# Kernel optimization log

Measured on AMD Instinct MI355X. Metric: run time of the kernel, lower is better.

The kernel has to match this reference:

```python
import jax, jax.numpy as jnp
import numpy as np

BZ, D_IN, D_STATE, D_OUT, L = 8, 256, 512, 256, 4096


def setup_inputs() -> dict:
    key = jax.random.key(0)
    k_u, k_a, k_b, k_c = jax.random.split(key, 4)
    init_scale = 0.5
    u = jax.random.normal(k_u, (BZ, D_IN, L), dtype=jnp.float32)
    A_unconstrained = jax.random.normal(k_a, (D_STATE,), dtype=jnp.float32) * 0.1
    B_mat = jax.random.normal(k_b, (D_STATE, D_IN), dtype=jnp.float32) * init_scale / np.sqrt(D_IN)
    C_mat = jax.random.normal(k_c, (D_OUT, D_STATE), dtype=jnp.float32) * init_scale / np.sqrt(D_STATE)
    D_mat = jnp.zeros((D_OUT, D_IN), dtype=jnp.float32)
    h0 = jnp.zeros((D_STATE,), dtype=jnp.float32)
    return {"u": u, "A_unconstrained": A_unconstrained, "B_mat": B_mat,
            "C_mat": C_mat, "D_mat": D_mat, "h0": h0}


def reference(u, A_unconstrained, B_mat, C_mat, D_mat, h0):
    # u: (B, input_dim, L)
    Bz = u.shape[0]
    A_diag = -jax.nn.softplus(A_unconstrained)          # (S,)
    # Precompute input projection for all timesteps: (L, B, S)
    Bu = jnp.einsum('bil,si->lbs', u, B_mat)
    state0 = jnp.broadcast_to(h0[None, :], (Bz, A_diag.shape[0]))

    def step(state, bu_t):
        x_t = state * A_diag[None, :] + bu_t            # (B, S)
        return x_t, x_t

    _, xs = jax.lax.scan(step, state0, Bu)              # xs: (L, B, S)
    # y_t = x_t @ C^T + u_t @ D^T, assembled as (B, output_dim, L)
    Y = jnp.einsum('lbs,os->bol', xs, C_mat) + jnp.einsum('bil,oi->bol', u, D_mat)
    return Y
```

## Files before the change

### kernel.cpp

```cpp
#include <hip/hip_runtime.h>
#include <math.h>

#define BZ 8
#define DI 256
#define DS 512
#define DOUT 256
#define LL 4096
#define BS (BZ * DS)
#define CH 64
#define CT 64
#define XST 520

typedef __bf16 bf16x8 __attribute__((ext_vector_type(8)));
typedef float f32x4 __attribute__((ext_vector_type(4)));
typedef unsigned short us8 __attribute__((ext_vector_type(8)));

#define WAITV(n) asm volatile("s_waitcnt vmcnt(" #n ")" ::: "memory")
#define WAITL0   asm volatile("s_waitcnt lgkmcnt(0)" ::: "memory")
#define SB0      __builtin_amdgcn_sched_barrier(0)

__device__ __forceinline__ ushort f2b(float f) {
    union { float f; unsigned u; } v; v.f = f;
    unsigned r = v.u + 0x7FFFu + ((v.u >> 16) & 1u);
    return (ushort)(r >> 16);
}
__device__ __forceinline__ float b2f(ushort h) {
    union { unsigned u; float f; } v; v.u = ((unsigned)h) << 16;
    return v.f;
}

__device__ __forceinline__ void gload16(const void* g, ushort* l) {
    __builtin_amdgcn_global_load_lds(
        (const __attribute__((address_space(1))) unsigned int*)g,
        (__attribute__((address_space(3))) unsigned int*)l,
        16, 0, 0);
}

__global__ __launch_bounds__(256) void k_prep(const float* __restrict__ Au,
                                              float* __restrict__ apow,
                                              const float* __restrict__ Bm,
                                              const float* __restrict__ Cm,
                                              ushort* __restrict__ Bmb,
                                              ushort* __restrict__ Cmb) {
    const int t = blockIdx.x * 256 + threadIdx.x;
    const int n1 = DS * DI / 4, n2 = DOUT * DS / 4;
    if (t < n1) {
        float4 v = ((const float4*)Bm)[t];
        ushort4 o; o.x = f2b(v.x); o.y = f2b(v.y); o.z = f2b(v.z); o.w = f2b(v.w);
        ((ushort4*)Bmb)[t] = o;
    } else if (t < n1 + n2) {
        float4 v = ((const float4*)Cm)[t - n1];
        ushort4 o; o.x = f2b(v.x); o.y = f2b(v.y); o.z = f2b(v.z); o.w = f2b(v.w);
        ((ushort4*)Cmb)[t - n1] = o;
    }
    if (t < DS) {
        float x = Au[t];
        float sp = (x > 15.f) ? x : log1pf(expf(x));
        float ad = -sp;
        float p = 1.f;
        apow[t] = 1.f;
        for (int j = 1; j <= CT; ++j) { p *= ad; apow[j * DS + t] = p; }
    }
}

__global__ __launch_bounds__(256) void k_finals(const float* __restrict__ u,
                                                const ushort* __restrict__ Bmb,
                                                const float* __restrict__ apow,
                                                float* __restrict__ finals) {
    __shared__ ushort smem[13312];
    const int tid = threadIdx.x;
    const int w = tid >> 6, lane = tid & 63;
    const int mrow = lane & 15, quad = lane >> 4;
    const int c0 = blockIdx.x, sg = blockIdx.y, b = blockIdx.z;
    const int s0 = sg * 128, l0 = c0 * 64;

    f32x4 acc[2][4];
#pragma unroll
    for (int mi = 0; mi < 2; ++mi)
#pragma unroll
        for (int ni = 0; ni < 4; ++ni) acc[mi][ni] = (f32x4)0.f;

    const float* usrc = u + ((size_t)b * DI + 4 * w + (lane >> 4)) * LL + l0 + (lane & 15) * 4;

    auto stageU = [&](int it) {
        const int bufu = (it & 1) * 4096;
        const float* s_ = usrc + (size_t)(it * 32) * LL;
        gload16(s_, smem + bufu + w * 512);
        gload16(s_ + (size_t)16 * LL, smem + bufu + w * 512 + 2048);
    };
    auto xposeU = [&](int it) {
        const float* uf = (const float*)&smem[(it & 1) * 4096];
        const int bto = 8192 + (it & 1) * 2560;
        float va[4], vb[4];
#pragma unroll
        for (int j = 0; j < 4; ++j) {
            va[j] = uf[(4 * w + j) * 64 + lane];
            vb[j] = uf[(16 + 4 * w + j) * 64 + lane];
        }
        ushort4 o1, o2;
        o1.x = f2b(va[0]); o1.y = f2b(va[1]); o1.z = f2b(va[2]); o1.w = f2b(va[3]);
        o2.x = f2b(vb[0]); o2.y = f2b(vb[1]); o2.z = f2b(vb[2]); o2.w = f2b(vb[3]);
        *(ushort4*)&smem[bto + lane * 40 + 4 * w] = o1;
        *(ushort4*)&smem[bto + lane * 40 + 16 + 4 * w] = o2;
    };

    stageU(0);
    __syncthreads();
#pragma unroll
    for (int it = 0; it < DI / 32; ++it) {
        if (it + 1 < DI / 32) stageU(it + 1);
        xposeU(it);
        __syncthreads();
        const int bto = 8192 + (it & 1) * 2560;
        bf16x8 bfr[4];
#pragma unroll
        for (int ni = 0; ni < 4; ++ni)
            bfr[ni] = *(const bf16x8*)&smem[bto + (ni * 16 + mrow) * 40 + quad * 8];
        bf16x8 af[2];
#pragma unroll
        for (int mi = 0; mi < 2; ++mi)
            af[mi] = *(const bf16x8*)&Bmb[(size_t)(s0 + 32 * w + mi * 16 + mrow) * DI + it * 32 + quad * 8];
#pragma unroll
        for (int mi = 0; mi < 2; ++mi)
#pragma unroll
            for (int ni = 0; ni < 4; ++ni)
                acc[mi][ni] = __builtin_amdgcn_mfma_f32_16x16x32_bf16(af[mi], bfr[ni], acc[mi][ni], 0, 0, 0);
        __syncthreads();
    }

    float F[2][4];
#pragma unroll
    for (int mi = 0; mi < 2; ++mi) {
        const int sb = s0 + 32 * w + mi * 16 + quad * 4;
        f32x4 a16 = *(const f32x4*)&apow[16 * DS + sb];
        f32x4 wgt = *(const f32x4*)&apow[(size_t)(15 - mrow) * DS + sb];
#pragma unroll
        for (int r = 0; r < 4; ++r) {
            float h = acc[mi][0][r];
            h = h * a16[r] + acc[mi][1][r];
            h = h * a16[r] + acc[mi][2][r];
            h = h * a16[r] + acc[mi][3][r];
            F[mi][r] = wgt[r] * h;
        }
    }
#pragma unroll
    for (int d = 1; d < 16; d <<= 1)
#pragma unroll
        for (int mi = 0; mi < 2; ++mi)
#pragma unroll
            for (int r = 0; r < 4; ++r)
                F[mi][r] += __shfl_xor(F[mi][r], d);
    if (mrow == 0) {
#pragma unroll
        for (int mi = 0; mi < 2; ++mi) {
            f32x4 o; o[0] = F[mi][0]; o[1] = F[mi][1]; o[2] = F[mi][2]; o[3] = F[mi][3];
            *(f32x4*)&finals[(size_t)c0 * BS + (size_t)b * DS + s0 + 32 * w + mi * 16 + quad * 4] = o;
        }
    }
}

__global__ __launch_bounds__(256, 2) void k_mainB(const float* __restrict__ u,
                                                  const ushort* __restrict__ Bmb,
                                                  const ushort* __restrict__ Cmb,
                                                  const float* __restrict__ apow,
                                                  const float* __restrict__ h0,
                                                  const float* __restrict__ finals,
                                                  float* __restrict__ Y) {
    __shared__ ushort smem[34304];
    float* crl = (float*)&smem[33280];
    const int tid = threadIdx.x;
    const int w = tid >> 6, lane = tid & 63;
    const int mrow = lane & 15, quad = lane >> 4;
    const int c0 = blockIdx.x, b = blockIdx.y;
    const int l0 = c0 * 64;

    const float* usrc = u + ((size_t)b * DI + 4 * w + (lane >> 4)) * LL + l0 + (lane & 15) * 4;

    auto stageU = [&](int it) {
        const int bufu = (it % 3) * 4096;
        const float* s_ = usrc + (size_t)(it * 32) * LL;
        gload16(s_, smem + bufu + w * 512);
        gload16(s_ + (size_t)16 * LL, smem + bufu + w * 512 + 2048);
    };
    auto xposeU = [&](int it) {
        const float* uf = (const float*)&smem[(it % 3) * 4096];
        const int bto = 12288 + (it & 1) * 2560;
        float va[4], vb[4];
#pragma unroll
        for (int j = 0; j < 4; ++j) {
            va[j] = uf[(4 * w + j) * 64 + lane];
            vb[j] = uf[(16 + 4 * w + j) * 64 + lane];
        }
        ushort4 o1, o2;
        o1.x = f2b(va[0]); o1.y = f2b(va[1]); o1.z = f2b(va[2]); o1.w = f2b(va[3]);
        o2.x = f2b(vb[0]); o2.y = f2b(vb[1]); o2.z = f2b(vb[2]); o2.w = f2b(vb[3]);
        *(ushort4*)&smem[bto + lane * 40 + 4 * w] = o1;
        *(ushort4*)&smem[bto + lane * 40 + 16 + 4 * w] = o2;
    };

    stageU(0); stageU(1);
    {
        const float aT0 = apow[CT * DS + tid];
        const float aT1 = apow[CT * DS + 256 + tid];
        float cva = h0[tid], cvb = h0[256 + tid];
        const float* fb = finals + (size_t)b * DS;
        int c = 0;
        for (; c + 8 <= c0; c += 8) {
            float fa[8], fc[8];
#pragma unroll
            for (int j = 0; j < 8; ++j) {
                fa[j] = fb[(size_t)(c + j) * BS + tid];
                fc[j] = fb[(size_t)(c + j) * BS + 256 + tid];
            }
#pragma unroll
            for (int j = 0; j < 8; ++j) {
                cva = aT0 * cva + fa[j];
                cvb = aT1 * cvb + fc[j];
            }
        }
        for (; c < c0; ++c) {
            cva = aT0 * cva + fb[(size_t)c * BS + tid];
            cvb = aT1 * cvb + fb[(size_t)c * BS + 256 + tid];
        }
        crl[tid] = cva; crl[256 + tid] = cvb;
    }

    f32x4 acc1[8][4];
#pragma unroll
    for (int mi = 0; mi < 8; ++mi)
#pragma unroll
        for (int ni = 0; ni < 4; ++ni) acc1[mi][ni] = (f32x4)0.f;

#pragma unroll
    for (int it = 0; it < DI / 32; ++it) {
        bf16x8 af[8];
#pragma unroll
        for (int mi = 0; mi < 8; ++mi)
            af[mi] = *(const bf16x8*)&Bmb[(size_t)(128 * w + mi * 16 + mrow) * DI + it * 32 + quad * 8];
        SB0;
        if (it + 2 < DI / 32) stageU(it + 2);
        if (it == 0) { WAITV(12); }
        xposeU(it);
        WAITL0;
        __builtin_amdgcn_s_barrier();
        SB0;
        const int bto = 12288 + (it & 1) * 2560;
        bf16x8 bfr[4];
#pragma unroll
        for (int ni = 0; ni < 4; ++ni)
            bfr[ni] = *(const bf16x8*)&smem[bto + (ni * 16 + mrow) * 40 + quad * 8];
#pragma unroll
        for (int mi = 0; mi < 8; ++mi)
#pragma unroll
            for (int ni = 0; ni < 4; ++ni)
                acc1[mi][ni] = __builtin_amdgcn_mfma_f32_16x16x32_bf16(af[mi], bfr[ni], acc1[mi][ni], 0, 0, 0);
        WAITL0;
        __builtin_amdgcn_s_barrier();
        SB0;
    }
    __syncthreads();

#pragma unroll
    for (int mi = 0; mi < 8; ++mi) {
        const int sloc = 128 * w + mi * 16 + quad * 4;
#pragma unroll
        for (int ni = 0; ni < 4; ++ni) {
            const int lloc = ni * 16 + mrow;
            f32x4 v = acc1[mi][ni];
            ushort4 o; o.x = f2b(v[0]); o.y = f2b(v[1]); o.z = f2b(v[2]); o.w = f2b(v[3]);
            *(ushort4*)&smem[lloc * XST + sloc] = o;
        }
    }
    __syncthreads();

    {
        const float2 av = *(const float2*)&apow[DS + 2 * tid];
        float x0 = 0.f, x1 = 0.f;
        unsigned* p = (unsigned*)&smem[2 * tid];
#pragma unroll 8
        for (int l = 0; l < CT; ++l) {
            unsigned v = p[l * (XST / 2)];
            x0 = av.x * x0 + b2f((ushort)(v & 0xFFFFu));
            x1 = av.y * x1 + b2f((ushort)(v >> 16));
            p[l * (XST / 2)] = (unsigned)f2b(x0) | ((unsigned)f2b(x1) << 16);
        }
    }
    __syncthreads();

    {
        const int lr = tid >> 2, g = tid & 3;
#pragma unroll
        for (int cc = 0; cc < 16; ++cc) {
            const int s = g * 128 + cc * 8;
            us8 x = *(const us8*)&smem[lr * XST + s];
            float4 a1 = *(const float4*)&apow[(size_t)(lr + 1) * DS + s];
            float4 a2 = *(const float4*)&apow[(size_t)(lr + 1) * DS + s + 4];
            float4 c1 = *(const float4*)&crl[s];
            float4 c2 = *(const float4*)&crl[s + 4];
            us8 o;
            o[0] = f2b(b2f(x[0]) + a1.x * c1.x);
            o[1] = f2b(b2f(x[1]) + a1.y * c1.y);
            o[2] = f2b(b2f(x[2]) + a1.z * c1.z);
            o[3] = f2b(b2f(x[3]) + a1.w * c1.w);
            o[4] = f2b(b2f(x[4]) + a2.x * c2.x);
            o[5] = f2b(b2f(x[5]) + a2.y * c2.y);
            o[6] = f2b(b2f(x[6]) + a2.z * c2.z);
            o[7] = f2b(b2f(x[7]) + a2.w * c2.w);
            *(us8*)&smem[lr * XST + s] = o;
        }
    }
    __syncthreads();

    f32x4 acc2[4][4];
#pragma unroll
    for (int mi = 0; mi < 4; ++mi)
#pragma unroll
        for (int ni = 0; ni < 4; ++ni) acc2[mi][ni] = (f32x4)0.f;

#pragma unroll
    for (int it = 0; it < DS / 32; ++it) {
        bf16x8 af2[4], bfr2[4];
#pragma unroll
        for (int mi = 0; mi < 4; ++mi)
            af2[mi] = *(const bf16x8*)&smem[(mi * 16 + mrow) * XST + it * 32 + quad * 8];
#pragma unroll
        for (int ni = 0; ni < 4; ++ni)
            bfr2[ni] = *(const bf16x8*)&Cmb[(size_t)(64 * w + ni * 16 + mrow) * DS + it * 32 + quad * 8];
#pragma unroll
        for (int mi = 0; mi < 4; ++mi)
#pragma unroll
            for (int ni = 0; ni < 4; ++ni)
                acc2[mi][ni] = __builtin_amdgcn_mfma_f32_16x16x32_bf16(af2[mi], bfr2[ni], acc2[mi][ni], 0, 0, 0);
    }

#pragma unroll
    for (int mi = 0; mi < 4; ++mi) {
        const int l = l0 + mi * 16 + quad * 4;
#pragma unroll
        for (int ni = 0; ni < 4; ++ni) {
            const int o = 64 * w + ni * 16 + mrow;
            *(float4*)&Y[((size_t)b * DOUT + o) * LL + l] = *(float4*)&acc2[mi][ni];
        }
    }
}

__global__ __launch_bounds__(256) void k_dadd(const float* __restrict__ Dm,
                                              const float* __restrict__ u,
                                              float* __restrict__ Y) {
    __shared__ int nz;
    if (threadIdx.x == 0) nz = 0;
    __syncthreads();
    const int o0 = blockIdx.x * 16;
    {
        const float4* dp = (const float4*)(Dm + (size_t)o0 * DI);
        int any = 0;
#pragma unroll
        for (int k = 0; k < 4; ++k) {
            float4 v = dp[threadIdx.x + k * 256];
            any |= (v.x != 0.f || v.y != 0.f || v.z != 0.f || v.w != 0.f);
        }
        if (any) atomicOr(&nz, 1);
    }
    __syncthreads();
    if (nz == 0) return;
    const int o = o0 + (threadIdx.x >> 4);
    const int li = threadIdx.x & 15;
    const int b = blockIdx.y;
    for (int lc = 0; lc < LL / 16; ++lc) {
        const int l = lc * 16 + li;
        float s = 0.f;
        for (int i = 0; i < DI; ++i)
            s += Dm[o * DI + i] * u[((size_t)b * DI + i) * LL + l];
        Y[((size_t)b * DOUT + o) * LL + l] += s;
    }
}

extern "C" void kernel_launch(void* const* d_in, const int* in_sizes, int n_in,
                              void* d_out, int out_size, void* d_ws, size_t ws_size,
                              hipStream_t stream) {
    const float* u  = (const float*)d_in[0];
    const float* Au = (const float*)d_in[1];
    const float* Bm = (const float*)d_in[2];
    const float* Cm = (const float*)d_in[3];
    const float* Dm = (const float*)d_in[4];
    const float* h0 = (const float*)d_in[5];
    float* Y = (float*)d_out;

    char* p = (char*)d_ws;
    float* finals  = (float*)p;  p += (size_t)CH * BS * 4;
    float* apow    = (float*)p;  p += (size_t)(CT + 1) * DS * 4;
    ushort* Bmb    = (ushort*)p; p += (size_t)DS * DI * 2;
    ushort* Cmb    = (ushort*)p; p += (size_t)DOUT * DS * 2;

    k_prep<<<dim3(256), 256, 0, stream>>>(Au, apow, Bm, Cm, Bmb, Cmb);
    k_finals<<<dim3(CH, DS / 128, BZ), 256, 0, stream>>>(u, Bmb, apow, finals);
    k_mainB<<<dim3(CH, BZ), 256, 0, stream>>>(u, Bmb, Cmb, apow, h0, finals, Y);
    k_dadd<<<dim3(DOUT / 16, BZ), 256, 0, stream>>>(Dm, u, Y);
}
```

Measured before the change: 163.3 us.

## Halve chunk length to 32 and restructure finals kernel to full-state tiles

The scan chunk length drops from 64 to 32 timesteps, which doubles the chunk count. k_mainB gets half-sized tiles and shared memory with higher occupancy, so the main kernel now runs 1024 blocks instead of 512. k_finals is reorganised so that each block covers all 512 states for a chunk, with a triple-buffered u pipeline and raw barriers replacing __syncthreads. The intra-chunk sequential scan is shorter and batches its LDS reads and writes in groups of 8. The cost is a longer serial prefix over finals in k_mainB (128 chunks instead of 64) and more finals traffic.

```diff
diff --git a/kernel.cpp b/kernel.cpp
--- a/kernel.cpp
+++ b/kernel.cpp
@@ -7,8 +7,8 @@
 #define DOUT 256
 #define LL 4096
 #define BS (BZ * DS)
-#define CH 64
-#define CT 64
+#define CH 128
+#define CT 32
 #define XST 520
 
 typedef __bf16 bf16x8 __attribute__((ext_vector_type(8)));
@@ -63,139 +63,123 @@
     }
 }
 
-__global__ __launch_bounds__(256) void k_finals(const float* __restrict__ u,
-                                                const ushort* __restrict__ Bmb,
-                                                const float* __restrict__ apow,
-                                                float* __restrict__ finals) {
-    __shared__ ushort smem[13312];
+__global__ __launch_bounds__(256, 4) void k_finals(const float* __restrict__ u,
+                                                   const ushort* __restrict__ Bmb,
+                                                   const float* __restrict__ apow,
+                                                   float* __restrict__ finals) {
+    __shared__ ushort smem[8704];
     const int tid = threadIdx.x;
     const int w = tid >> 6, lane = tid & 63;
     const int mrow = lane & 15, quad = lane >> 4;
-    const int c0 = blockIdx.x, sg = blockIdx.y, b = blockIdx.z;
-    const int s0 = sg * 128, l0 = c0 * 64;
-
-    f32x4 acc[2][4];
-#pragma unroll
-    for (int mi = 0; mi < 2; ++mi)
-#pragma unroll
-        for (int ni = 0; ni < 4; ++ni) acc[mi][ni] = (f32x4)0.f;
-
-    const float* usrc = u + ((size_t)b * DI + 4 * w + (lane >> 4)) * LL + l0 + (lane & 15) * 4;
+    const int c0 = blockIdx.x, b = blockIdx.y;
+    const int l0 = c0 * CT;
+
+    f32x4 acc[8][2];
+#pragma unroll
+    for (int mi = 0; mi < 8; ++mi)
+#pragma unroll
+        for (int ni = 0; ni < 2; ++ni) acc[mi][ni] = (f32x4)0.f;
+
+    const float* usrc = u + ((size_t)b * DI + (tid >> 3)) * LL + l0 + (tid & 7) * 4;
 
     auto stageU = [&](int it) {
-        const int bufu = (it & 1) * 4096;
-        const float* s_ = usrc + (size_t)(it * 32) * LL;
-        gload16(s_, smem + bufu + w * 512);
-        gload16(s_ + (size_t)16 * LL, smem + bufu + w * 512 + 2048);
+        gload16(usrc + (size_t)(it * 32) * LL, smem + (it % 3) * 2048 + w * 512);
     };
     auto xposeU = [&](int it) {
-        const float* uf = (const float*)&smem[(it & 1) * 4096];
-        const int bto = 8192 + (it & 1) * 2560;
-        float va[4], vb[4];
-#pragma unroll
-        for (int j = 0; j < 4; ++j) {
-            va[j] = uf[(4 * w + j) * 64 + lane];
-            vb[j] = uf[(16 + 4 * w + j) * 64 + lane];
-        }
-        ushort4 o1, o2;
-        o1.x = f2b(va[0]); o1.y = f2b(va[1]); o1.z = f2b(va[2]); o1.w = f2b(va[3]);
-        o2.x = f2b(vb[0]); o2.y = f2b(vb[1]); o2.z = f2b(vb[2]); o2.w = f2b(vb[3]);
-        *(ushort4*)&smem[bto + lane * 40 + 4 * w] = o1;
-        *(ushort4*)&smem[bto + lane * 40 + 16 + 4 * w] = o2;
+        const float* uf = (const float*)&smem[(it % 3) * 2048];
+        const int bto = 6144 + (it & 1) * 1280;
+        const int r0 = 8 * w + (lane >> 5) * 4, cl = lane & 31;
+        float v[4];
+#pragma unroll
+        for (int j = 0; j < 4; ++j) v[j] = uf[(r0 + j) * 32 + cl];
+        ushort4 o; o.x = f2b(v[0]); o.y = f2b(v[1]); o.z = f2b(v[2]); o.w = f2b(v[3]);
+        *(ushort4*)&smem[bto + cl * 40 + r0] = o;
     };
 
-    stageU(0);
-    __syncthreads();
+    stageU(0); stageU(1);
 #pragma unroll
     for (int it = 0; it < DI / 32; ++it) {
-        if (it + 1 < DI / 32) stageU(it + 1);
+        bf16x8 af[8];
+#pragma unroll
+        for (int mi = 0; mi < 8; ++mi)
+            af[mi] = *(const bf16x8*)&Bmb[(size_t)(128 * w + mi * 16 + mrow) * DI + it * 32 + quad * 8];
+        SB0;
+        if (it + 2 < DI / 32) stageU(it + 2);
+        if (it == 0) { WAITV(10); }
         xposeU(it);
-        __syncthreads();
-        const int bto = 8192 + (it & 1) * 2560;
-        bf16x8 bfr[4];
-#pragma unroll
-        for (int ni = 0; ni < 4; ++ni)
+        WAITL0;
+        __builtin_amdgcn_s_barrier();
+        SB0;
+        const int bto = 6144 + (it & 1) * 1280;
+        bf16x8 bfr[2];
+#pragma unroll
+        for (int ni = 0; ni < 2; ++ni)
             bfr[ni] = *(const bf16x8*)&smem[bto + (ni * 16 + mrow) * 40 + quad * 8];
-        bf16x8 af[2];
-#pragma unroll
-        for (int mi = 0; mi < 2; ++mi)
-            af[mi] = *(const bf16x8*)&Bmb[(size_t)(s0 + 32 * w + mi * 16 + mrow) * DI + it * 32 + quad * 8];
-#pragma unroll
-        for (int mi = 0; mi < 2; ++mi)
-#pragma unroll
-            for (int ni = 0; ni < 4; ++ni)
+#pragma unroll
+        for (int mi = 0; mi < 8; ++mi)
+#pragma unroll
+            for (int ni = 0; ni < 2; ++ni)
                 acc[mi][ni] = __builtin_amdgcn_mfma_f32_16x16x32_bf16(af[mi], bfr[ni], acc[mi][ni], 0, 0, 0);
-        __syncthreads();
-    }
-
-    float F[2][4];
-#pragma unroll
-    for (int mi = 0; mi < 2; ++mi) {
-        const int sb = s0 + 32 * w + mi * 16 + quad * 4;
+        WAITL0;
+        __builtin_amdgcn_s_barrier();
+        SB0;
+    }
+
+    float F[8][4];
+#pragma unroll
+    for (int mi = 0; mi < 8; ++mi) {
+        const int sb = 128 * w + mi * 16 + quad * 4;
         f32x4 a16 = *(const f32x4*)&apow[16 * DS + sb];
         f32x4 wgt = *(const f32x4*)&apow[(size_t)(15 - mrow) * DS + sb];
 #pragma unroll
-        for (int r = 0; r < 4; ++r) {
-            float h = acc[mi][0][r];
-            h = h * a16[r] + acc[mi][1][r];
-            h = h * a16[r] + acc[mi][2][r];
-            h = h * a16[r] + acc[mi][3][r];
-            F[mi][r] = wgt[r] * h;
-        }
+        for (int r = 0; r < 4; ++r)
+            F[mi][r] = wgt[r] * (acc[mi][0][r] * a16[r] + acc[mi][1][r]);
     }
 #pragma unroll
     for (int d = 1; d < 16; d <<= 1)
 #pragma unroll
-        for (int mi = 0; mi < 2; ++mi)
+        for (int mi = 0; mi < 8; ++mi)
 #pragma unroll
             for (int r = 0; r < 4; ++r)
                 F[mi][r] += __shfl_xor(F[mi][r], d);
     if (mrow == 0) {
 #pragma unroll
-        for (int mi = 0; mi < 2; ++mi) {
+        for (int mi = 0; mi < 8; ++mi) {
             f32x4 o; o[0] = F[mi][0]; o[1] = F[mi][1]; o[2] = F[mi][2]; o[3] = F[mi][3];
-            *(f32x4*)&finals[(size_t)c0 * BS + (size_t)b * DS + s0 + 32 * w + mi * 16 + quad * 4] = o;
-        }
-    }
-}
-
-__global__ __launch_bounds__(256, 2) void k_mainB(const float* __restrict__ u,
+            *(f32x4*)&finals[(size_t)c0 * BS + (size_t)b * DS + 128 * w + mi * 16 + quad * 4] = o;
+        }
+    }
+}
+
+__global__ __launch_bounds__(256, 4) void k_mainB(const float* __restrict__ u,
                                                   const ushort* __restrict__ Bmb,
                                                   const ushort* __restrict__ Cmb,
                                                   const float* __restrict__ apow,
                                                   const float* __restrict__ h0,
                                                   const float* __restrict__ finals,
                                                   float* __restrict__ Y) {
-    __shared__ ushort smem[34304];
-    float* crl = (float*)&smem[33280];
+    __shared__ ushort smem[17664];
+    float* crl = (float*)&smem[16640];
     const int tid = threadIdx.x;
     const int w = tid >> 6, lane = tid & 63;
     const int mrow = lane & 15, quad = lane >> 4;
     const int c0 = blockIdx.x, b = blockIdx.y;
-    const int l0 = c0 * 64;
-
-    const float* usrc = u + ((size_t)b * DI + 4 * w + (lane >> 4)) * LL + l0 + (lane & 15) * 4;
+    const int l0 = c0 * CT;
+
+    const float* usrc = u + ((size_t)b * DI + (tid >> 3)) * LL + l0 + (tid & 7) * 4;
 
     auto stageU = [&](int it) {
-        const int bufu = (it % 3) * 4096;
-        const float* s_ = usrc + (size_t)(it * 32) * LL;
-        gload16(s_, smem + bufu + w * 512);
-        gload16(s_ + (size_t)16 * LL, smem + bufu + w * 512 + 2048);
+        gload16(usrc + (size_t)(it * 32) * LL, smem + (it % 3) * 2048 + w * 512);
     };
     auto xposeU = [&](int it) {
-        const float* uf = (const float*)&smem[(it % 3) * 4096];
-        const int bto = 12288 + (it & 1) * 2560;
-        float va[4], vb[4];
-#pragma unroll
-        for (int j = 0; j < 4; ++j) {
-            va[j] = uf[(4 * w + j) * 64 + lane];
-            vb[j] = uf[(16 + 4 * w + j) * 64 + lane];
-        }
-        ushort4 o1, o2;
-        o1.x = f2b(va[0]); o1.y = f2b(va[1]); o1.z = f2b(va[2]); o1.w = f2b(va[3]);
-        o2.x = f2b(vb[0]); o2.y = f2b(vb[1]); o2.z = f2b(vb[2]); o2.w = f2b(vb[3]);
-        *(ushort4*)&smem[bto + lane * 40 + 4 * w] = o1;
-        *(ushort4*)&smem[bto + lane * 40 + 16 + 4 * w] = o2;
+        const float* uf = (const float*)&smem[(it % 3) * 2048];
+        const int bto = 6144 + (it & 1) * 1280;
+        const int r0 = 8 * w + (lane >> 5) * 4, cl = lane & 31;
+        float v[4];
+#pragma unroll
+        for (int j = 0; j < 4; ++j) v[j] = uf[(r0 + j) * 32 + cl];
+        ushort4 o; o.x = f2b(v[0]); o.y = f2b(v[1]); o.z = f2b(v[2]); o.w = f2b(v[3]);
+        *(ushort4*)&smem[bto + cl * 40 + r0] = o;
     };
 
     stageU(0); stageU(1);
@@ -225,11 +209,11 @@
         crl[tid] = cva; crl[256 + tid] = cvb;
     }
 
-    f32x4 acc1[8][4];
+    f32x4 acc1[8][2];
 #pragma unroll
     for (int mi = 0; mi < 8; ++mi)
 #pragma unroll
-        for (int ni = 0; ni < 4; ++ni) acc1[mi][ni] = (f32x4)0.f;
+        for (int ni = 0; ni < 2; ++ni) acc1[mi][ni] = (f32x4)0.f;
 
 #pragma unroll
     for (int it = 0; it < DI / 32; ++it) {
@@ -239,20 +223,20 @@
             af[mi] = *(const bf16x8*)&Bmb[(size_t)(128 * w + mi * 16 + mrow) * DI + it * 32 + quad * 8];
         SB0;
         if (it + 2 < DI / 32) stageU(it + 2);
-        if (it == 0) { WAITV(12); }
+        if (it == 0) { WAITV(10); }
         xposeU(it);
         WAITL0;
         __builtin_amdgcn_s_barrier();
         SB0;
-        const int bto = 12288 + (it & 1) * 2560;
-        bf16x8 bfr[4];
-#pragma unroll
-        for (int ni = 0; ni < 4; ++ni)
+        const int bto = 6144 + (it & 1) * 1280;
+        bf16x8 bfr[2];
+#pragma unroll
+        for (int ni = 0; ni < 2; ++ni)
             bfr[ni] = *(const bf16x8*)&smem[bto + (ni * 16 + mrow) * 40 + quad * 8];
 #pragma unroll
         for (int mi = 0; mi < 8; ++mi)
 #pragma unroll
-            for (int ni = 0; ni < 4; ++ni)
+            for (int ni = 0; ni < 2; ++ni)
                 acc1[mi][ni] = __builtin_amdgcn_mfma_f32_16x16x32_bf16(af[mi], bfr[ni], acc1[mi][ni], 0, 0, 0);
         WAITL0;
         __builtin_amdgcn_s_barrier();
@@ -264,7 +248,7 @@
     for (int mi = 0; mi < 8; ++mi) {
         const int sloc = 128 * w + mi * 16 + quad * 4;
 #pragma unroll
-        for (int ni = 0; ni < 4; ++ni) {
+        for (int ni = 0; ni < 2; ++ni) {
             const int lloc = ni * 16 + mrow;
             f32x4 v = acc1[mi][ni];
             ushort4 o; o.x = f2b(v[0]); o.y = f2b(v[1]); o.z = f2b(v[2]); o.w = f2b(v[3]);
@@ -276,22 +260,29 @@
     {
         const float2 av = *(const float2*)&apow[DS + 2 * tid];
         float x0 = 0.f, x1 = 0.f;
-        unsigned* p = (unsigned*)&smem[2 * tid];
-#pragma unroll 8
-        for (int l = 0; l < CT; ++l) {
-            unsigned v = p[l * (XST / 2)];
-            x0 = av.x * x0 + b2f((ushort)(v & 0xFFFFu));
-            x1 = av.y * x1 + b2f((ushort)(v >> 16));
-            p[l * (XST / 2)] = (unsigned)f2b(x0) | ((unsigned)f2b(x1) << 16);
+        unsigned* pp = (unsigned*)&smem[2 * tid];
+#pragma unroll
+        for (int bt = 0; bt < CT / 8; ++bt) {
+            unsigned v[8];
+#pragma unroll
+            for (int j = 0; j < 8; ++j) v[j] = pp[(bt * 8 + j) * (XST / 2)];
+#pragma unroll
+            for (int j = 0; j < 8; ++j) {
+                x0 = av.x * x0 + b2f((ushort)(v[j] & 0xFFFFu));
+                x1 = av.y * x1 + b2f((ushort)(v[j] >> 16));
+                v[j] = (unsigned)f2b(x0) | ((unsigned)f2b(x1) << 16);
+            }
+#pragma unroll
+            for (int j = 0; j < 8; ++j) pp[(bt * 8 + j) * (XST / 2)] = v[j];
         }
     }
     __syncthreads();
 
     {
-        const int lr = tid >> 2, g = tid & 3;
-#pragma unroll
-        for (int cc = 0; cc < 16; ++cc) {
-            const int s = g * 128 + cc * 8;
+        const int lr = tid >> 3, g = tid & 7;
+#pragma unroll
+        for (int cc = 0; cc < 8; ++cc) {
+            const int s = g * 64 + cc * 8;
             us8 x = *(const us8*)&smem[lr * XST + s];
             float4 a1 = *(const float4*)&apow[(size_t)(lr + 1) * DS + s];
             float4 a2 = *(const float4*)&apow[(size_t)(lr + 1) * DS + s + 4];
@@ -311,30 +302,30 @@
     }
     __syncthreads();
 
-    f32x4 acc2[4][4];
-#pragma unroll
-    for (int mi = 0; mi < 4; ++mi)
+    f32x4 acc2[2][4];
+#pragma unroll
+    for (int mi = 0; mi < 2; ++mi)
 #pragma unroll
         for (int ni = 0; ni < 4; ++ni) acc2[mi][ni] = (f32x4)0.f;
 
 #pragma unroll
     for (int it = 0; it < DS / 32; ++it) {
-        bf16x8 af2[4], bfr2[4];
-#pragma unroll
-        for (int mi = 0; mi < 4; ++mi)
+        bf16x8 af2[2], bfr2[4];
+#pragma unroll
+        for (int mi = 0; mi < 2; ++mi)
             af2[mi] = *(const bf16x8*)&smem[(mi * 16 + mrow) * XST + it * 32 + quad * 8];
 #pragma unroll
         for (int ni = 0; ni < 4; ++ni)
             bfr2[ni] = *(const bf16x8*)&Cmb[(size_t)(64 * w + ni * 16 + mrow) * DS + it * 32 + quad * 8];
 #pragma unroll
-        for (int mi = 0; mi < 4; ++mi)
+        for (int mi = 0; mi < 2; ++mi)
 #pragma unroll
             for (int ni = 0; ni < 4; ++ni)
                 acc2[mi][ni] = __builtin_amdgcn_mfma_f32_16x16x32_bf16(af2[mi], bfr2[ni], acc2[mi][ni], 0, 0, 0);
     }
 
 #pragma unroll
-    for (int mi = 0; mi < 4; ++mi) {
+    for (int mi = 0; mi < 2; ++mi) {
         const int l = l0 + mi * 16 + quad * 4;
 #pragma unroll
         for (int ni = 0; ni < 4; ++ni) {
@@ -393,7 +384,7 @@
     ushort* Cmb    = (ushort*)p; p += (size_t)DOUT * DS * 2;
 
     k_prep<<<dim3(256), 256, 0, stream>>>(Au, apow, Bm, Cm, Bmb, Cmb);
-    k_finals<<<dim3(CH, DS / 128, BZ), 256, 0, stream>>>(u, Bmb, apow, finals);
+    k_finals<<<dim3(CH, BZ), 256, 0, stream>>>(u, Bmb, apow, finals);
     k_mainB<<<dim3(CH, BZ), 256, 0, stream>>>(u, Bmb, Cmb, apow, h0, finals, Y);
     k_dadd<<<dim3(DOUT / 16, BZ), 256, 0, stream>>>(Dm, u, Y);
 }
```

After: 235.0 us. +43.9%, slower.
